# Performance work log

Hardware: AMD Instinct MI355X
Metric: run time of the kernel (lower is better)

## Reference

```python
import jax, jax.numpy as jnp
import numpy as np

N_NODES = 50000
N_RAND_EDGES = 800000
N_GRAPHS = 64
IN_DIM, HID, HEADS = 1024, 64, 4
NEG_SLOPE = 0.2  # PyG GATConv default


def setup_inputs() -> dict:
    key = jax.random.key(0)
    ks = jax.random.split(key, 16)
    x = jax.random.normal(ks[0], (N_NODES, IN_DIM), dtype=jnp.float32)
    src = jax.random.randint(ks[1], (N_RAND_EDGES,), 0, N_NODES, dtype=jnp.int32)
    dst = jax.random.randint(ks[2], (N_RAND_EDGES,), 0, N_NODES, dtype=jnp.int32)
    loop = jnp.arange(N_NODES, dtype=jnp.int32)
    # PyG GATConv adds self-loops by default; bake them into edge_index.
    edge_index = jnp.stack([jnp.concatenate([src, loop]), jnp.concatenate([dst, loop])])
    batch = jnp.sort(jax.random.randint(ks[3], (N_NODES,), 0, N_GRAPHS, dtype=jnp.int32))
    s = 0.05
    W1 = jax.random.normal(ks[4], (IN_DIM, HEADS * HID), dtype=jnp.float32) * s
    att_src1 = jax.random.normal(ks[5], (HEADS, HID), dtype=jnp.float32) * s
    att_dst1 = jax.random.normal(ks[6], (HEADS, HID), dtype=jnp.float32) * s
    b1 = jnp.zeros((HEADS * HID,), dtype=jnp.float32)
    W2 = jax.random.normal(ks[7], (HEADS * HID, HID), dtype=jnp.float32) * s
    att_src2 = jax.random.normal(ks[8], (1, HID), dtype=jnp.float32) * s
    att_dst2 = jax.random.normal(ks[9], (1, HID), dtype=jnp.float32) * s
    b2 = jnp.zeros((HID,), dtype=jnp.float32)
    fc_w = jax.random.normal(ks[10], (HID, 2), dtype=jnp.float32) * s
    fc_b = jnp.zeros((2,), dtype=jnp.float32)
    return {"x": x, "edge_index": edge_index, "batch": batch,
            "W1": W1, "att_src1": att_src1, "att_dst1": att_dst1, "b1": b1,
            "W2": W2, "att_src2": att_src2, "att_dst2": att_dst2, "b2": b2,
            "fc_w": fc_w, "fc_b": fc_b}


def gat_conv(x, src, dst, W, a_src, a_dst, b):
    """PyG GATConv (eval mode, concat=True). x:[N,Fin] -> [N, H*C]."""
    N = x.shape[0]
    H, C = a_src.shape
    h = (x @ W).reshape(N, H, C)                      # [N,H,C]
    al_s = jnp.einsum('nhc,hc->nh', h, a_src)         # [N,H]
    al_d = jnp.einsum('nhc,hc->nh', h, a_dst)
    e = jax.nn.leaky_relu(al_s[src] + al_d[dst], NEG_SLOPE)   # [E,H]
    # segment-softmax over edges grouped by destination node
    m = jax.ops.segment_max(e, dst, num_segments=N)           # [N,H]
    w = jnp.exp(e - m[dst])
    denom = jax.ops.segment_sum(w, dst, num_segments=N)
    alpha = w / denom[dst]                                    # [E,H]
    msg = h[src] * alpha[:, :, None]                          # [E,H,C]
    out = jax.ops.segment_sum(msg, dst, num_segments=N)       # [N,H,C]
    return out.reshape(N, H * C) + b


def reference(x, edge_index, batch, W1, att_src1, att_dst1, b1,
              W2, att_src2, att_dst2, b2, fc_w, fc_b):
    src, dst = edge_index[0], edge_index[1]
    # dropout is identity in eval mode
    h = jax.nn.elu(gat_conv(x, src, dst, W1, att_src1, att_dst1, b1))
    h = jax.nn.elu(gat_conv(h, src, dst, W2, att_src2, att_dst2, b2))
    # global mean pool over graphs
    sums = jax.ops.segment_sum(h, batch, num_segments=N_GRAPHS)          # [G,HID]
    cnt = jax.ops.segment_sum(jnp.ones((h.shape[0],), h.dtype), batch,
                              num_segments=N_GRAPHS)
    pooled = sums / jnp.maximum(cnt, 1.0)[:, None]
    return pooled @ fc_w + fc_b                                          # [G,2]
```

## Files before the change

### kernel.cpp

```cpp
#include <hip/hip_runtime.h>
#include <hip/hip_bf16.h>

#define NNODES   50000
#define NGRAPHS  64
#define INDIM    1024
#define HIDC     64
#define HEADS1   4
#define F1       (HEADS1*HIDC)
#define NEG_SLOPE 0.2f

#define WS_COUNTS   0
#define WS_ZEROLEN  50000
#define WS_INDPTR   54208
#define WS_CURSOR   104256
#define WS_CSRSRC   154304
#define WS_CSRDST   1004304
#define WS_BSUM     1854304
#define WS_ALS1     1854368
#define WS_ALD1     2054368
#define WS_ALS2     2254368
#define WS_ALD2     2304368
#define WS_BP       2354368
#define WS_BP2      2485440
#define WS_H1B      2493632
#define WS_X2B      8893632
#define WS_H2B      15293632
#define WS_HFIN     16893632

typedef __attribute__((ext_vector_type(8))) short bf16x8;
typedef __attribute__((ext_vector_type(4))) float f32x4;

__device__ __forceinline__ ushort f2bf(float f) {
    union { float f; uint u; } v; v.f = f;
    uint r = v.u + 0x7fff + ((v.u >> 16) & 1);
    return (ushort)(r >> 16);
}
__device__ __forceinline__ float bf2f(ushort u) {
    union { uint u; float f; } v; v.u = (uint)u << 16; return v.f;
}

__global__ void prep_kernel(const float* __restrict__ W1, const float* __restrict__ W2,
                            ushort* __restrict__ Bp1, ushort* __restrict__ Bp2,
                            int* __restrict__ counts) {
    int b = blockIdx.x;
    int tid = threadIdx.x;
    if (b < 1024) {
        int o = b * 256 + tid;
        int j = o & 7;
        int lane = (o >> 3) & 63;
        int kchunk = (o >> 9) & 31;
        int ntile = o >> 14;
        int k = kchunk * 32 + (lane >> 4) * 8 + j;
        int n = ntile * 16 + (lane & 15);
        Bp1[o] = f2bf(W1[k * 256 + n]);
    } else if (b < 1088) {
        int o = (b - 1024) * 256 + tid;
        int j = o & 7;
        int lane = (o >> 3) & 63;
        int kchunk = (o >> 9) & 7;
        int ntile = o >> 12;
        int k = kchunk * 32 + (lane >> 4) * 8 + j;
        int n = ntile * 16 + (lane & 15);
        Bp2[o] = f2bf(W2[k * 64 + n]);
    } else {
        int i = (b - 1088) * 256 + tid;
        if (i < NNODES) counts[i] = 0;
    }
}

__global__ void hist_kernel(const int* __restrict__ dst, int* __restrict__ counts, int E) {
    int i = blockIdx.x * blockDim.x + threadIdx.x;
    if (i < E) atomicAdd(&counts[dst[i]], 1);
}

__global__ __launch_bounds__(1024) void scan1_kernel(const int* __restrict__ counts,
                                                     int* __restrict__ indptr,
                                                     int* __restrict__ bsum, int N) {
    __shared__ int sm[1024];
    int b = blockIdx.x;
    int i = b * 1024 + (int)threadIdx.x;
    int v = (i < N) ? counts[i] : 0;
    sm[threadIdx.x] = v;
    __syncthreads();
    for (int off = 1; off < 1024; off <<= 1) {
        int t = (threadIdx.x >= (unsigned)off) ? sm[threadIdx.x - off] : 0;
        __syncthreads();
        sm[threadIdx.x] += t;
        __syncthreads();
    }
    if (i < N) indptr[i + 1] = sm[threadIdx.x];
    if (threadIdx.x == 1023) bsum[b] = sm[1023];
}

__global__ void scan2_kernel(int* __restrict__ bsum, int nb) {
    int lane = threadIdx.x;
    int v = (lane < nb) ? bsum[lane] : 0;
    int orig = v;
    #pragma unroll
    for (int off = 1; off < 64; off <<= 1) {
        int t = __shfl_up(v, off, 64);
        if (lane >= off) v += t;
    }
    if (lane < nb) bsum[lane] = v - orig;
}

__global__ __launch_bounds__(1024) void scan3_kernel(const int* __restrict__ counts,
                                                     int* __restrict__ indptr,
                                                     int* __restrict__ cursor,
                                                     const int* __restrict__ bsum, int N) {
    int i = blockIdx.x * 1024 + (int)threadIdx.x;
    if (i == 0) indptr[0] = 0;
    if (i < N) {
        int incl = indptr[i + 1] + bsum[blockIdx.x];
        indptr[i + 1] = incl;
        cursor[i] = incl - counts[i];
    }
}

__global__ void fill_kernel(const int* __restrict__ src, const int* __restrict__ dst,
                            int* __restrict__ cursor, int* __restrict__ csr_src, int E) {
    int i = blockIdx.x * blockDim.x + threadIdx.x;
    if (i < E) {
        int d = dst[i];
        int pos = atomicAdd(&cursor[d], 1);
        csr_src[pos] = src[i];
    }
}

__global__ __launch_bounds__(256) void gemm1_mfma(const float* __restrict__ A,
                                                  const ushort* __restrict__ Bp,
                                                  ushort* __restrict__ C,
                                                  const float* __restrict__ asrc,
                                                  const float* __restrict__ adst,
                                                  float* __restrict__ als,
                                                  float* __restrict__ ald,
                                                  int M) {
    __shared__ __align__(16) ushort Atile[2][64 * 32];
    const int K = 1024, N = 256;
    int tid = threadIdx.x;
    int lane = tid & 63;
    int w = tid >> 6;
    int wm = w >> 1, wn = w & 1;
    int m0 = blockIdx.x * 64;

    const float* srow[2];
    int soff[2];
    #pragma unroll
    for (int l = 0; l < 2; ++l) {
        int slot = l * 256 + tid;
        int m = slot >> 3, hc = slot & 7;
        int c = hc >> 1;
        int row = m0 + m; if (row >= M) row = M - 1;
        srow[l] = A + (size_t)row * K + hc * 4;
        soff[l] = (m * 4 + (c ^ ((m >> 1) & 3))) * 8 + (hc & 1) * 4;
    }
    int afrag_off[2];
    #pragma unroll
    for (int mt = 0; mt < 2; ++mt) {
        int r = wm * 32 + mt * 16 + (lane & 15);
        int cq = lane >> 4;
        afrag_off[mt] = (r * 4 + (cq ^ ((r >> 1) & 3))) * 8;
    }
    const ushort* bbase[8];
    #pragma unroll
    for (int nt = 0; nt < 8; ++nt) {
        int ntile = wn * 8 + nt;
        bbase[nt] = Bp + ((size_t)(ntile * 32) * 64 + lane) * 8;
    }

    f32x4 acc[2][8] = {};
    float4 v[2];
    #pragma unroll
    for (int l = 0; l < 2; ++l) v[l] = *(const float4*)(srow[l]);

    for (int kc = 0; kc < 32; ++kc) {
        ushort* At = Atile[kc & 1];
        #pragma unroll
        for (int l = 0; l < 2; ++l) {
            ushort4 b;
            b.x = f2bf(v[l].x); b.y = f2bf(v[l].y);
            b.z = f2bf(v[l].z); b.w = f2bf(v[l].w);
            *(ushort4*)&At[soff[l]] = b;
        }
        __syncthreads();
        if (kc < 31) {
            #pragma unroll
            for (int l = 0; l < 2; ++l)
                v[l] = *(const float4*)(srow[l] + (kc + 1) * 32);
        }
        bf16x8 afr[2];
        #pragma unroll
        for (int mt = 0; mt < 2; ++mt)
            afr[mt] = *(const bf16x8*)&At[afrag_off[mt]];
        #pragma unroll
        for (int nt = 0; nt < 8; ++nt) {
            bf16x8 bfr = *(const bf16x8*)(bbase[nt] + (size_t)kc * 64 * 8);
            #pragma unroll
            for (int mt = 0; mt < 2; ++mt)
                acc[mt][nt] = __builtin_amdgcn_mfma_f32_16x16x32_bf16(afr[mt], bfr, acc[mt][nt], 0, 0, 0);
        }
    }

    float a_s[8], a_d[8];
    #pragma unroll
    for (int nt = 0; nt < 8; ++nt) {
        int col = wn * 128 + nt * 16 + (lane & 15);
        a_s[nt] = asrc[col];
        a_d[nt] = adst[col];
    }
    #pragma unroll
    for (int mt = 0; mt < 2; ++mt) {
        #pragma unroll
        for (int nt = 0; nt < 8; ++nt) {
            int col = wn * 128 + nt * 16 + (lane & 15);
            #pragma unroll
            for (int r = 0; r < 4; ++r) {
                int row = m0 + wm * 32 + mt * 16 + (lane >> 4) * 4 + r;
                if (row < M) C[(size_t)row * N + col] = f2bf(acc[mt][nt][r]);
            }
        }
        #pragma unroll
        for (int hg = 0; hg < 2; ++hg) {
            int head = wn * 2 + hg;
            #pragma unroll
            for (int r = 0; r < 4; ++r) {
                int row = m0 + wm * 32 + mt * 16 + (lane >> 4) * 4 + r;
                float s = 0.f, d = 0.f;
                #pragma unroll
                for (int q = 0; q < 4; ++q) {
                    float c = acc[mt][4 * hg + q][r];
                    s = fmaf(c, a_s[4 * hg + q], s);
                    d = fmaf(c, a_d[4 * hg + q], d);
                }
                #pragma unroll
                for (int off = 1; off < 16; off <<= 1) {
                    s += __shfl_xor(s, off, 64);
                    d += __shfl_xor(d, off, 64);
                }
                if ((lane & 15) == 0 && row < M) {
                    als[row * 4 + head] = s;
                    ald[row * 4 + head] = d;
                }
            }
        }
    }
}

__global__ __launch_bounds__(256) void gemm2_mfma(const ushort* __restrict__ Ab,
                                                  const ushort* __restrict__ Bp,
                                                  ushort* __restrict__ C,
                                                  const float* __restrict__ asrc,
                                                  const float* __restrict__ adst,
                                                  float* __restrict__ als,
                                                  float* __restrict__ ald,
                                                  int M) {
    int tid = threadIdx.x;
    int lane = tid & 63;
    int w = tid >> 6;
    int m0 = blockIdx.x * 64 + w * 16;

    f32x4 acc[4] = {};
    #pragma unroll 2
    for (int kc = 0; kc < 8; ++kc) {
        int r = m0 + (lane & 15);
        if (r >= M) r = M - 1;
        bf16x8 afr = *(const bf16x8*)&Ab[(size_t)r * 256 + kc * 32 + (lane >> 4) * 8];
        #pragma unroll
        for (int nt = 0; nt < 4; ++nt) {
            bf16x8 bfr = *(const bf16x8*)&Bp[((nt * 8 + kc) * 64 + lane) * 8];
            acc[nt] = __builtin_amdgcn_mfma_f32_16x16x32_bf16(afr, bfr, acc[nt], 0, 0, 0);
        }
    }
    float a_s[4], a_d[4];
    #pragma unroll
    for (int nt = 0; nt < 4; ++nt) {
        a_s[nt] = asrc[nt * 16 + (lane & 15)];
        a_d[nt] = adst[nt * 16 + (lane & 15)];
    }
    #pragma unroll
    for (int nt = 0; nt < 4; ++nt) {
        int col = nt * 16 + (lane & 15);
        #pragma unroll
        for (int r = 0; r < 4; ++r) {
            int row = m0 + (lane >> 4) * 4 + r;
            if (row < M) C[(size_t)row * 64 + col] = f2bf(acc[nt][r]);
        }
    }
    #pragma unroll
    for (int r = 0; r < 4; ++r) {
        int row = m0 + (lane >> 4) * 4 + r;
        float s = 0.f, d = 0.f;
        #pragma unroll
        for (int nt = 0; nt < 4; ++nt) {
            float c = acc[nt][r];
            s = fmaf(c, a_s[nt], s);
            d = fmaf(c, a_d[nt], d);
        }
        #pragma unroll
        for (int off = 1; off < 16; off <<= 1) {
            s += __shfl_xor(s, off, 64);
            d += __shfl_xor(d, off, 64);
        }
        if ((lane & 15) == 0 && row < M) {
            als[row] = s;
            ald[row] = d;
        }
    }
}

__device__ __forceinline__ float wave_reduce_sum(float v) {
    #pragma unroll
    for (int off = 32; off > 0; off >>= 1) v += __shfl_xor(v, off, 64);
    return v;
}

__device__ __forceinline__ float edge_w(float e) {
    e = (e > 0.f) ? e : NEG_SLOPE * e;
    return __expf(e);
}

__global__ __launch_bounds__(256) void agg1_kernel(const ushort* __restrict__ h,
                                                   const float* __restrict__ als,
                                                   const float* __restrict__ ald,
                                                   const int* __restrict__ indptr,
                                                   const int* __restrict__ csr_src,
                                                   const float* __restrict__ bias,
                                                   ushort* __restrict__ out, int N) {
    __shared__ int   s_s[4][64];
    __shared__ float s_w[4][64][4];
    int wv   = threadIdx.x >> 6;
    int lane = threadIdx.x & 63;
    int n = blockIdx.x * 4 + wv;
    if (n >= N) return;
    int hd = lane >> 4;
    int beg = indptr[n], end = indptr[n + 1];
    float4 aldv = *(const float4*)&ald[n * 4];

    float4 acc = make_float4(0.f, 0.f, 0.f, 0.f);
    float den = 0.f;

    for (int base = beg; base < end; base += 64) {
        int cnt = end - base; if (cnt > 64) cnt = 64;
        if (lane < cnt) {
            int s = csr_src[base + lane];
            s_s[wv][lane] = s;
            float4 av = *(const float4*)&als[s * 4];
            s_w[wv][lane][0] = edge_w(av.x + aldv.x);
            s_w[wv][lane][1] = edge_w(av.y + aldv.y);
            s_w[wv][lane][2] = edge_w(av.z + aldv.z);
            s_w[wv][lane][3] = edge_w(av.w + aldv.w);
        }
        #pragma unroll 4
        for (int e = 0; e < cnt; ++e) {
            int s = s_s[wv][e];
            float wt = s_w[wv][e][hd];
            ushort4 a = *(const ushort4*)&h[(size_t)s * 256 + lane * 4];
            acc.x = fmaf(wt, bf2f(a.x), acc.x);
            acc.y = fmaf(wt, bf2f(a.y), acc.y);
            acc.z = fmaf(wt, bf2f(a.z), acc.z);
            acc.w = fmaf(wt, bf2f(a.w), acc.w);
            den += wt;
        }
    }

    float inv = 1.0f / den;
    float4 bv = *(const float4*)&bias[lane * 4];
    float o0 = acc.x * inv + bv.x, o1 = acc.y * inv + bv.y;
    float o2 = acc.z * inv + bv.z, o3 = acc.w * inv + bv.w;
    o0 = (o0 > 0.f) ? o0 : (__expf(o0) - 1.0f);
    o1 = (o1 > 0.f) ? o1 : (__expf(o1) - 1.0f);
    o2 = (o2 > 0.f) ? o2 : (__expf(o2) - 1.0f);
    o3 = (o3 > 0.f) ? o3 : (__expf(o3) - 1.0f);
    ushort4 ob; ob.x = f2bf(o0); ob.y = f2bf(o1); ob.z = f2bf(o2); ob.w = f2bf(o3);
    *(ushort4*)&out[(size_t)n * 256 + lane * 4] = ob;
}

__global__ __launch_bounds__(256) void agg2_kernel(const ushort* __restrict__ h,
                                                   const float* __restrict__ als,
                                                   const float* __restrict__ ald,
                                                   const int* __restrict__ indptr,
                                                   const int* __restrict__ csr_src,
                                                   const float* __restrict__ bias,
                                                   float* __restrict__ out, int N) {
    __shared__ int   s_s[8][32];
    __shared__ float s_w[8][32];
    int tid = threadIdx.x;
    int sl  = tid >> 5;
    int l32 = tid & 31;
    int n = blockIdx.x * 8 + sl;
    if (n >= N) return;
    int beg = indptr[n], end = indptr[n + 1];
    float ald_n = ald[n];

    float2 acc = make_float2(0.f, 0.f);
    float den = 0.f;

    for (int base = beg; base < end; base += 32) {
        int cnt = end - base; if (cnt > 32) cnt = 32;
        if (l32 < cnt) {
            int s = csr_src[base + l32];
            s_s[sl][l32] = s;
            s_w[sl][l32] = edge_w(als[s] + ald_n);
        }
        #pragma unroll 4
        for (int e = 0; e < cnt; ++e) {
            int s = s_s[sl][e];
            float wt = s_w[sl][e];
            ushort2 hv = *(const ushort2*)&h[(size_t)s * 64 + l32 * 2];
            acc.x = fmaf(wt, bf2f(hv.x), acc.x);
            acc.y = fmaf(wt, bf2f(hv.y), acc.y);
            den += wt;
        }
    }

    float inv = 1.0f / den;
    float o0 = acc.x * inv + bias[l32 * 2];
    float o1 = acc.y * inv + bias[l32 * 2 + 1];
    o0 = (o0 > 0.f) ? o0 : (__expf(o0) - 1.0f);
    o1 = (o1 > 0.f) ? o1 : (__expf(o1) - 1.0f);
    *(float2*)&out[(size_t)n * 64 + l32 * 2] = make_float2(o0, o1);
}

__global__ __launch_bounds__(256) void pool_fc_kernel(const float* __restrict__ hfin,
                                                      const int* __restrict__ batch,
                                                      const float* __restrict__ fc_w,
                                                      const float* __restrict__ fc_b,
                                                      float* __restrict__ out, int N) {
    __shared__ float lacc[4][64];
    int g = blockIdx.x;
    int beg, end;
    {
        int lo = 0, hi = N;
        while (lo < hi) { int mid = (lo + hi) >> 1; if (batch[mid] < g) lo = mid + 1; else hi = mid; }
        beg = lo;
        lo = beg; hi = N;
        while (lo < hi) { int mid = (lo + hi) >> 1; if (batch[mid] < g + 1) lo = mid + 1; else hi = mid; }
        end = lo;
    }
    int lane = threadIdx.x & 63;
    int wv = threadIdx.x >> 6;
    float acc = 0.f;
    for (int n = beg + wv; n < end; n += 4)
        acc += hfin[(size_t)n * 64 + lane];
    lacc[wv][lane] = acc;
    __syncthreads();
    if (wv == 0) {
        float s = lacc[0][lane] + lacc[1][lane] + lacc[2][lane] + lacc[3][lane];
        float cnt = fmaxf((float)(end - beg), 1.0f);
        float pooled = s / cnt;
        float p0 = wave_reduce_sum(pooled * fc_w[lane * 2 + 0]);
        float p1 = wave_reduce_sum(pooled * fc_w[lane * 2 + 1]);
        if (lane == 0) {
            out[g * 2 + 0] = p0 + fc_b[0];
            out[g * 2 + 1] = p1 + fc_b[1];
        }
    }
}

extern "C" void kernel_launch(void* const* d_in, const int* in_sizes, int n_in,
                              void* d_out, int out_size, void* d_ws, size_t ws_size,
                              hipStream_t stream) {
    const float* x      = (const float*)d_in[0];
    const int*   ei     = (const int*)d_in[1];
    const int*   batch  = (const int*)d_in[2];
    const float* W1     = (const float*)d_in[3];
    const float* asrc1  = (const float*)d_in[4];
    const float* adst1  = (const float*)d_in[5];
    const float* b1     = (const float*)d_in[6];
    const float* W2     = (const float*)d_in[7];
    const float* asrc2  = (const float*)d_in[8];
    const float* adst2  = (const float*)d_in[9];
    const float* b2     = (const float*)d_in[10];
    const float* fc_w   = (const float*)d_in[11];
    const float* fc_b   = (const float*)d_in[12];
    float* out          = (float*)d_out;

    const int N = in_sizes[2];
    const int E = in_sizes[1] / 2;
    const int* src = ei;
    const int* dst = ei + E;

    float* ws = (float*)d_ws;
    int*    counts  = (int*)(ws + WS_COUNTS);
    int*    indptr  = (int*)(ws + WS_INDPTR);
    int*    cursor  = (int*)(ws + WS_CURSOR);
    int*    csr_src = (int*)(ws + WS_CSRSRC);
    int*    bsum    = (int*)(ws + WS_BSUM);
    float*  al_s1   = ws + WS_ALS1;
    float*  al_d1   = ws + WS_ALD1;
    float*  al_s2   = ws + WS_ALS2;
    float*  al_d2   = ws + WS_ALD2;
    ushort* bp      = (ushort*)(ws + WS_BP);
    ushort* bp2     = (ushort*)(ws + WS_BP2);
    ushort* h1b     = (ushort*)(ws + WS_H1B);
    ushort* x2b     = (ushort*)(ws + WS_X2B);
    ushort* h2b     = (ushort*)(ws + WS_H2B);
    float*  hfin    = ws + WS_HFIN;

    const int nb = (N + 1023) / 1024;

    prep_kernel<<<1284, 256, 0, stream>>>(W1, W2, bp, bp2, counts);
    hist_kernel<<<(E + 255) / 256, 256, 0, stream>>>(dst, counts, E);
    scan1_kernel<<<nb, 1024, 0, stream>>>(counts, indptr, bsum, N);
    scan2_kernel<<<1, 64, 0, stream>>>(bsum, nb);
    scan3_kernel<<<nb, 1024, 0, stream>>>(counts, indptr, cursor, bsum, N);
    fill_kernel<<<(E + 255) / 256, 256, 0, stream>>>(src, dst, cursor, csr_src, E);
    gemm1_mfma<<<(N + 63) / 64, 256, 0, stream>>>(
        x, bp, h1b, asrc1, adst1, al_s1, al_d1, N);
    agg1_kernel<<<(N + 3) / 4, 256, 0, stream>>>(h1b, al_s1, al_d1, indptr, csr_src, b1, x2b, N);
    gemm2_mfma<<<(N + 63) / 64, 256, 0, stream>>>(
        x2b, bp2, h2b, asrc2, adst2, al_s2, al_d2, N);
    agg2_kernel<<<(N + 7) / 8, 256, 0, stream>>>(h2b, al_s2, al_d2, indptr, csr_src, b2, hfin, N);
    pool_fc_kernel<<<NGRAPHS, 256, 0, stream>>>(hfin, batch, fc_w, fc_b, out, N);
}
```

Baseline: 602.4 us.

## Restructure gemm1 with direct global-to-LDS async loads and per-wave full-N tiles

Rewrites the first-layer GEMM so that each wave owns 32 rows and all 256 output columns, with 128 rows per block. The fp32 A tile is streamed straight into a swizzled, double-buffered per-wave LDS region using global_load_lds, with explicit vmcnt waits in place of block-wide barriers. The fp32-to-bf16 conversion moves to fragment-read time. This aims to overlap A loading with MFMA and to drop the register round-trip and __syncthreads, but it doubles the accumulator registers (launch bounds 256,2), which may limit occupancy.

```diff
diff --git a/kernel.cpp b/kernel.cpp
--- a/kernel.cpp
+++ b/kernel.cpp
@@ -29,6 +29,9 @@
 
 typedef __attribute__((ext_vector_type(8))) short bf16x8;
 typedef __attribute__((ext_vector_type(4))) float f32x4;
+
+typedef __attribute__((address_space(1))) const unsigned int cgu32;
+typedef __attribute__((address_space(3))) unsigned int su32;
 
 __device__ __forceinline__ ushort f2bf(float f) {
     union { float f; uint u; } v; v.f = f;
@@ -127,7 +130,7 @@
     }
 }
 
-__global__ __launch_bounds__(256) void gemm1_mfma(const float* __restrict__ A,
+__global__ __launch_bounds__(256, 2) void gemm1_mfma(const float* __restrict__ A,
                                                   const ushort* __restrict__ Bp,
                                                   ushort* __restrict__ C,
                                                   const float* __restrict__ asrc,
@@ -135,96 +138,106 @@
                                                   float* __restrict__ als,
                                                   float* __restrict__ ald,
                                                   int M) {
-    __shared__ __align__(16) ushort Atile[2][64 * 32];
+    __shared__ __align__(16) float As[4][2][1024];
     const int K = 1024, N = 256;
     int tid = threadIdx.x;
     int lane = tid & 63;
     int w = tid >> 6;
-    int wm = w >> 1, wn = w & 1;
-    int m0 = blockIdx.x * 64;
-
-    const float* srow[2];
-    int soff[2];
-    #pragma unroll
-    for (int l = 0; l < 2; ++l) {
-        int slot = l * 256 + tid;
-        int m = slot >> 3, hc = slot & 7;
-        int c = hc >> 1;
-        int row = m0 + m; if (row >= M) row = M - 1;
-        srow[l] = A + (size_t)row * K + hc * 4;
-        soff[l] = (m * 4 + (c ^ ((m >> 1) & 3))) * 8 + (hc & 1) * 4;
-    }
-    int afrag_off[2];
+    int m0 = blockIdx.x * 128 + w * 32;
+
+    const float* gsrc[4];
+    #pragma unroll
+    for (int j = 0; j < 4; ++j) {
+        int prow = j * 8 + (lane >> 3);
+        int grow = m0 + prow; if (grow >= M) grow = M - 1;
+        int kswz = ((lane & 7) ^ (lane >> 3)) << 2;
+        gsrc[j] = A + (size_t)grow * K + kswz;
+    }
+    char* sbase = (char*)&As[w][0][0];
+
+    int aoff[2][2];
     #pragma unroll
     for (int mt = 0; mt < 2; ++mt) {
-        int r = wm * 32 + mt * 16 + (lane & 15);
-        int cq = lane >> 4;
-        afrag_off[mt] = (r * 4 + (cq ^ ((r >> 1) & 3))) * 8;
-    }
-    const ushort* bbase[8];
-    #pragma unroll
-    for (int nt = 0; nt < 8; ++nt) {
-        int ntile = wn * 8 + nt;
-        bbase[nt] = Bp + ((size_t)(ntile * 32) * 64 + lane) * 8;
-    }
-
-    f32x4 acc[2][8] = {};
-    float4 v[2];
-    #pragma unroll
-    for (int l = 0; l < 2; ++l) v[l] = *(const float4*)(srow[l]);
-
-    for (int kc = 0; kc < 32; ++kc) {
-        ushort* At = Atile[kc & 1];
-        #pragma unroll
-        for (int l = 0; l < 2; ++l) {
-            ushort4 b;
-            b.x = f2bf(v[l].x); b.y = f2bf(v[l].y);
-            b.z = f2bf(v[l].z); b.w = f2bf(v[l].w);
-            *(ushort4*)&At[soff[l]] = b;
-        }
-        __syncthreads();
-        if (kc < 31) {
-            #pragma unroll
-            for (int l = 0; l < 2; ++l)
-                v[l] = *(const float4*)(srow[l] + (kc + 1) * 32);
-        }
-        bf16x8 afr[2];
-        #pragma unroll
-        for (int mt = 0; mt < 2; ++mt)
-            afr[mt] = *(const bf16x8*)&At[afrag_off[mt]];
-        #pragma unroll
-        for (int nt = 0; nt < 8; ++nt) {
-            bf16x8 bfr = *(const bf16x8*)(bbase[nt] + (size_t)kc * 64 * 8);
-            #pragma unroll
-            for (int mt = 0; mt < 2; ++mt)
-                acc[mt][nt] = __builtin_amdgcn_mfma_f32_16x16x32_bf16(afr[mt], bfr, acc[mt][nt], 0, 0, 0);
-        }
-    }
-
-    float a_s[8], a_d[8];
-    #pragma unroll
-    for (int nt = 0; nt < 8; ++nt) {
-        int col = wn * 128 + nt * 16 + (lane & 15);
+        int lr = mt * 16 + (lane & 15);
+        int kq = lane >> 4;
+        #pragma unroll
+        for (int h = 0; h < 2; ++h)
+            aoff[mt][h] = lr * 128 + ((kq * 32 + h * 16) ^ ((lr & 7) << 4));
+    }
+
+    f32x4 acc[2][16] = {};
+
+    #pragma unroll
+    for (int j = 0; j < 4; ++j)
+        __builtin_amdgcn_global_load_lds((cgu32*)(gsrc[j]),
+                                         (su32*)(sbase + j * 1024 + lane * 16), 16, 0, 0);
+
+    #define G1_BLOADS(kc_)                                                          \
+        bf16x8 bfr[16];                                                             \
+        _Pragma("unroll")                                                           \
+        for (int nt = 0; nt < 16; ++nt)                                             \
+            bfr[nt] = *(const bf16x8*)&Bp[((size_t)(nt * 32 + (kc_)) * 64 + lane) * 8];
+    #define G1_FRAGS_MFMA(kc_)                                                      \
+        const char* sb = sbase + ((kc_) & 1) * 4096;                                \
+        bf16x8 afr[2];                                                              \
+        _Pragma("unroll")                                                           \
+        for (int mt = 0; mt < 2; ++mt) {                                            \
+            float4 fa = *(const float4*)(sb + aoff[mt][0]);                         \
+            float4 fb = *(const float4*)(sb + aoff[mt][1]);                         \
+            bf16x8 t;                                                               \
+            t[0] = (short)f2bf(fa.x); t[1] = (short)f2bf(fa.y);                     \
+            t[2] = (short)f2bf(fa.z); t[3] = (short)f2bf(fa.w);                     \
+            t[4] = (short)f2bf(fb.x); t[5] = (short)f2bf(fb.y);                     \
+            t[6] = (short)f2bf(fb.z); t[7] = (short)f2bf(fb.w);                     \
+            afr[mt] = t;                                                            \
+        }                                                                           \
+        _Pragma("unroll")                                                           \
+        for (int nt = 0; nt < 16; ++nt) {                                           \
+            acc[0][nt] = __builtin_amdgcn_mfma_f32_16x16x32_bf16(afr[0], bfr[nt], acc[0][nt], 0, 0, 0); \
+            acc[1][nt] = __builtin_amdgcn_mfma_f32_16x16x32_bf16(afr[1], bfr[nt], acc[1][nt], 0, 0, 0); \
+        }
+
+    for (int kc = 0; kc < 31; ++kc) {
+        G1_BLOADS(kc);
+        char* sn = sbase + ((kc + 1) & 1) * 4096;
+        #pragma unroll
+        for (int j = 0; j < 4; ++j)
+            __builtin_amdgcn_global_load_lds((cgu32*)(gsrc[j] + (kc + 1) * 32),
+                                             (su32*)(sn + j * 1024 + lane * 16), 16, 0, 0);
+        asm volatile("s_waitcnt vmcnt(4)" ::: "memory");
+        G1_FRAGS_MFMA(kc);
+    }
+    {
+        G1_BLOADS(31);
+        asm volatile("s_waitcnt vmcnt(0)" ::: "memory");
+        G1_FRAGS_MFMA(31);
+    }
+    #undef G1_BLOADS
+    #undef G1_FRAGS_MFMA
+
+    float a_s[16], a_d[16];
+    #pragma unroll
+    for (int nt = 0; nt < 16; ++nt) {
+        int col = nt * 16 + (lane & 15);
         a_s[nt] = asrc[col];
         a_d[nt] = adst[col];
     }
     #pragma unroll
     for (int mt = 0; mt < 2; ++mt) {
         #pragma unroll
-        for (int nt = 0; nt < 8; ++nt) {
-            int col = wn * 128 + nt * 16 + (lane & 15);
+        for (int nt = 0; nt < 16; ++nt) {
+            int col = nt * 16 + (lane & 15);
             #pragma unroll
             for (int r = 0; r < 4; ++r) {
-                int row = m0 + wm * 32 + mt * 16 + (lane >> 4) * 4 + r;
+                int row = m0 + mt * 16 + (lane >> 4) * 4 + r;
                 if (row < M) C[(size_t)row * N + col] = f2bf(acc[mt][nt][r]);
             }
         }
         #pragma unroll
-        for (int hg = 0; hg < 2; ++hg) {
-            int head = wn * 2 + hg;
+        for (int hg = 0; hg < 4; ++hg) {
             #pragma unroll
             for (int r = 0; r < 4; ++r) {
-                int row = m0 + wm * 32 + mt * 16 + (lane >> 4) * 4 + r;
+                int row = m0 + mt * 16 + (lane >> 4) * 4 + r;
                 float s = 0.f, d = 0.f;
                 #pragma unroll
                 for (int q = 0; q < 4; ++q) {
@@ -238,8 +251,8 @@
                     d += __shfl_xor(d, off, 64);
                 }
                 if ((lane & 15) == 0 && row < M) {
-                    als[row * 4 + head] = s;
-                    ald[row * 4 + head] = d;
+                    als[row * 4 + hg] = s;
+                    ald[row * 4 + hg] = d;
                 }
             }
         }
@@ -505,7 +518,7 @@
     scan2_kernel<<<1, 64, 0, stream>>>(bsum, nb);
     scan3_kernel<<<nb, 1024, 0, stream>>>(counts, indptr, cursor, bsum, N);
     fill_kernel<<<(E + 255) / 256, 256, 0, stream>>>(src, dst, cursor, csr_src, E);
-    gemm1_mfma<<<(N + 63) / 64, 256, 0, stream>>>(
+    gemm1_mfma<<<(N + 127) / 128, 256, 0, stream>>>(
         x, bp, h1b, asrc1, adst1, al_s1, al_d1, N);
     agg1_kernel<<<(N + 3) / 4, 256, 0, stream>>>(h1b, al_s1, al_d1, indptr, csr_src, b1, x2b, N);
     gemm2_mfma<<<(N + 63) / 64, 256, 0, stream>>>(
```

Result: no change. 602.0 us (-0.1%).

## Stage GEMM1 A and B tiles into LDS via async global_load_lds

Applied to the files above, without the earlier changes.

Rewrites the first-layer GEMM main loop so both the fp32 A tile and the pre-packed bf16 B tile are copied into double-buffered shared memory with direct global-to-LDS loads, overlapping the next chunk's fetch with the current chunk's MFMAs. The fp32-to-bf16 conversion moves to after the LDS read and uses packed convert instructions. An XOR swizzle on A is meant to avoid bank conflicts, and launch bounds request 3 blocks per CU. The cost is larger LDS use per block (fp32 A plus B buffers), which may limit occupancy, and the barrier placement relies on the async loads having completed.

```diff
diff --git a/kernel.cpp b/kernel.cpp
--- a/kernel.cpp
+++ b/kernel.cpp
@@ -30,6 +30,9 @@
 typedef __attribute__((ext_vector_type(8))) short bf16x8;
 typedef __attribute__((ext_vector_type(4))) float f32x4;
 
+typedef __attribute__((address_space(1))) const unsigned int cgu32;
+typedef __attribute__((address_space(3))) unsigned int su32;
+
 __device__ __forceinline__ ushort f2bf(float f) {
     union { float f; uint u; } v; v.f = f;
     uint r = v.u + 0x7fff + ((v.u >> 16) & 1);
@@ -37,6 +40,11 @@
 }
 __device__ __forceinline__ float bf2f(ushort u) {
     union { uint u; float f; } v; v.u = (uint)u << 16; return v.f;
+}
+__device__ __forceinline__ uint cvtpk(float lo, float hi) {
+    uint r;
+    asm("v_cvt_pk_bf16_f32 %0, %1, %2" : "=v"(r) : "v"(lo), "v"(hi));
+    return r;
 }
 
 __global__ void prep_kernel(const float* __restrict__ W1, const float* __restrict__ W2,
@@ -127,7 +135,7 @@
     }
 }
 
-__global__ __launch_bounds__(256) void gemm1_mfma(const float* __restrict__ A,
+__global__ __launch_bounds__(256, 3) void gemm1_mfma(const float* __restrict__ A,
                                                   const ushort* __restrict__ Bp,
                                                   ushort* __restrict__ C,
                                                   const float* __restrict__ asrc,
@@ -135,7 +143,8 @@
                                                   float* __restrict__ als,
                                                   float* __restrict__ ald,
                                                   int M) {
-    __shared__ __align__(16) ushort Atile[2][64 * 32];
+    __shared__ __align__(16) float  As[2][2048];
+    __shared__ __align__(16) ushort Bs[2][8192];
     const int K = 1024, N = 256;
     int tid = threadIdx.x;
     int lane = tid & 63;
@@ -143,63 +152,82 @@
     int wm = w >> 1, wn = w & 1;
     int m0 = blockIdx.x * 64;
 
-    const float* srow[2];
-    int soff[2];
-    #pragma unroll
-    for (int l = 0; l < 2; ++l) {
-        int slot = l * 256 + tid;
-        int m = slot >> 3, hc = slot & 7;
-        int c = hc >> 1;
-        int row = m0 + m; if (row >= M) row = M - 1;
-        srow[l] = A + (size_t)row * K + hc * 4;
-        soff[l] = (m * 4 + (c ^ ((m >> 1) & 3))) * 8 + (hc & 1) * 4;
-    }
-    int afrag_off[2];
+    const float* gsrcA[2];
+    #pragma unroll
+    for (int j = 0; j < 2; ++j) {
+        int gidx = j * 256 + tid;
+        int r = gidx >> 3, c = gidx & 7;
+        int grow = m0 + r; if (grow >= M) grow = M - 1;
+        gsrcA[j] = A + (size_t)grow * K + ((c ^ (r & 7)) << 2);
+    }
+    const ushort* gsrcB[4];
+    #pragma unroll
+    for (int j = 0; j < 4; ++j) {
+        int nt = j * 4 + w;
+        gsrcB[j] = Bp + (size_t)nt * 16384 + lane * 8;
+    }
+
+    int aoffA[2][2];
     #pragma unroll
     for (int mt = 0; mt < 2; ++mt) {
-        int r = wm * 32 + mt * 16 + (lane & 15);
-        int cq = lane >> 4;
-        afrag_off[mt] = (r * 4 + (cq ^ ((r >> 1) & 3))) * 8;
-    }
-    const ushort* bbase[8];
-    #pragma unroll
-    for (int nt = 0; nt < 8; ++nt) {
-        int ntile = wn * 8 + nt;
-        bbase[nt] = Bp + ((size_t)(ntile * 32) * 64 + lane) * 8;
-    }
+        int row = wm * 32 + mt * 16 + (lane & 15);
+        int kq = lane >> 4;
+        aoffA[mt][0] = row * 128 + (((kq * 2)     ^ (row & 7)) << 4);
+        aoffA[mt][1] = row * 128 + (((kq * 2 + 1) ^ (row & 7)) << 4);
+    }
+    int boff[8];
+    #pragma unroll
+    for (int nt = 0; nt < 8; ++nt)
+        boff[nt] = (wn * 8 + nt) * 1024 + lane * 16;
 
     f32x4 acc[2][8] = {};
-    float4 v[2];
-    #pragma unroll
-    for (int l = 0; l < 2; ++l) v[l] = *(const float4*)(srow[l]);
-
-    for (int kc = 0; kc < 32; ++kc) {
-        ushort* At = Atile[kc & 1];
-        #pragma unroll
-        for (int l = 0; l < 2; ++l) {
-            ushort4 b;
-            b.x = f2bf(v[l].x); b.y = f2bf(v[l].y);
-            b.z = f2bf(v[l].z); b.w = f2bf(v[l].w);
-            *(ushort4*)&At[soff[l]] = b;
-        }
+
+    auto STAGE = [&](int buf, int kc) {
+        char* da = (char*)As[buf];
+        char* db = (char*)Bs[buf];
+        #pragma unroll
+        for (int j = 0; j < 2; ++j)
+            __builtin_amdgcn_global_load_lds((cgu32*)(gsrcA[j] + kc * 32),
+                                             (su32*)(da + j * 4096 + tid * 16), 16, 0, 0);
+        #pragma unroll
+        for (int j = 0; j < 4; ++j)
+            __builtin_amdgcn_global_load_lds((cgu32*)(gsrcB[j] + kc * 512),
+                                             (su32*)(db + j * 4096 + tid * 16), 16, 0, 0);
+    };
+    auto COMPUTE = [&](int buf) {
+        const char* sa = (const char*)As[buf];
+        const char* sb = (const char*)Bs[buf];
+        bf16x8 afr[2];
+        #pragma unroll
+        for (int mt = 0; mt < 2; ++mt) {
+            float4 fa = *(const float4*)(sa + aoffA[mt][0]);
+            float4 fb = *(const float4*)(sa + aoffA[mt][1]);
+            union { uint u[4]; bf16x8 v; } p;
+            p.u[0] = cvtpk(fa.x, fa.y);
+            p.u[1] = cvtpk(fa.z, fa.w);
+            p.u[2] = cvtpk(fb.x, fb.y);
+            p.u[3] = cvtpk(fb.z, fb.w);
+            afr[mt] = p.v;
+        }
+        bf16x8 bfr[8];
+        #pragma unroll
+        for (int nt = 0; nt < 8; ++nt)
+            bfr[nt] = *(const bf16x8*)(sb + boff[nt]);
+        #pragma unroll
+        for (int nt = 0; nt < 8; ++nt) {
+            acc[0][nt] = __builtin_amdgcn_mfma_f32_16x16x32_bf16(afr[0], bfr[nt], acc[0][nt], 0, 0, 0);
+            acc[1][nt] = __builtin_amdgcn_mfma_f32_16x16x32_bf16(afr[1], bfr[nt], acc[1][nt], 0, 0, 0);
+        }
+    };
+
+    STAGE(0, 0);
+    __syncthreads();
+    for (int kc = 0; kc < 31; ++kc) {
+        STAGE((kc + 1) & 1, kc + 1);
+        COMPUTE(kc & 1);
         __syncthreads();
-        if (kc < 31) {
-            #pragma unroll
-            for (int l = 0; l < 2; ++l)
-                v[l] = *(const float4*)(srow[l] + (kc + 1) * 32);
-        }
-        bf16x8 afr[2];
-        #pragma unroll
-        for (int mt = 0; mt < 2; ++mt)
-            afr[mt] = *(const bf16x8*)&At[afrag_off[mt]];
-        #pragma unroll
-        for (int nt = 0; nt < 8; ++nt) {
-            bf16x8 bfr = *(const bf16x8*)(bbase[nt] + (size_t)kc * 64 * 8);
-            #pragma unroll
-            for (int mt = 0; mt < 2; ++mt)
-                acc[mt][nt] = __builtin_amdgcn_mfma_f32_16x16x32_bf16(afr[mt], bfr, acc[mt][nt], 0, 0, 0);
-        }
-    }
+    }
+    COMPUTE(1);
 
     float a_s[8], a_d[8];
     #pragma unroll
```

Result: no change. 613.7 us (+1.9%).

## Restructure gemm1 A staging into 128-wide K slabs with deeper prefetch

Applied to the files above, without the earlier changes.

gemm1 now stages 128-wide K slabs of A into double-buffered LDS, using an XOR swizzle and packed bf16 conversion via v_cvt_pk_bf16_f32. Global loads are prefetched two groups ahead, and synchronisation uses raw s_barrier only once per 4 k-steps. This is meant to cut barrier count and conversion instructions and to hide more global latency. It costs more registers (16 float4 prefetch buffers) with launch_bounds set to 2 blocks per SM, and 32KB of LDS. The aggregation kernels also raise their edge-loop unroll from 4 to 8.

```diff
diff --git a/kernel.cpp b/kernel.cpp
--- a/kernel.cpp
+++ b/kernel.cpp
@@ -38,6 +38,12 @@
 __device__ __forceinline__ float bf2f(ushort u) {
     union { uint u; float f; } v; v.u = (uint)u << 16; return v.f;
 }
+__device__ __forceinline__ uint cvtpk(float lo, float hi) {
+    uint r;
+    asm("v_cvt_pk_bf16_f32 %0, %1, %2" : "=v"(r) : "v"(lo), "v"(hi));
+    return r;
+}
+#define RAW_BARRIER() asm volatile("s_waitcnt lgkmcnt(0)\n\ts_barrier" ::: "memory")
 
 __global__ void prep_kernel(const float* __restrict__ W1, const float* __restrict__ W2,
                             ushort* __restrict__ Bp1, ushort* __restrict__ Bp2,
@@ -127,7 +133,7 @@
     }
 }
 
-__global__ __launch_bounds__(256) void gemm1_mfma(const float* __restrict__ A,
+__global__ __launch_bounds__(256, 2) void gemm1_mfma(const float* __restrict__ A,
                                                   const ushort* __restrict__ Bp,
                                                   ushort* __restrict__ C,
                                                   const float* __restrict__ asrc,
@@ -135,7 +141,7 @@
                                                   float* __restrict__ als,
                                                   float* __restrict__ ald,
                                                   int M) {
-    __shared__ __align__(16) ushort Atile[2][64 * 32];
+    __shared__ __align__(16) ushort Asl[2][64 * 128];
     const int K = 1024, N = 256;
     int tid = threadIdx.x;
     int lane = tid & 63;
@@ -143,63 +149,88 @@
     int wm = w >> 1, wn = w & 1;
     int m0 = blockIdx.x * 64;
 
-    const float* srow[2];
-    int soff[2];
-    #pragma unroll
-    for (int l = 0; l < 2; ++l) {
-        int slot = l * 256 + tid;
-        int m = slot >> 3, hc = slot & 7;
-        int c = hc >> 1;
-        int row = m0 + m; if (row >= M) row = M - 1;
-        srow[l] = A + (size_t)row * K + hc * 4;
-        soff[l] = (m * 4 + (c ^ ((m >> 1) & 3))) * 8 + (hc & 1) * 4;
-    }
-    int afrag_off[2];
+    int rloc = tid >> 2, q = tid & 3;
+    int grow = m0 + rloc; if (grow >= M) grow = M - 1;
+    const float* gA = A + (size_t)grow * K + q * 32;
+
+    char* abase = (char*)&Asl[0][0];
+    int woff[4];
+    #pragma unroll
+    for (int j = 0; j < 4; ++j)
+        woff[j] = rloc * 256 + (((q * 4 + j) ^ (rloc & 15)) << 4);
+
+    int aoff[2][4];
     #pragma unroll
     for (int mt = 0; mt < 2; ++mt) {
         int r = wm * 32 + mt * 16 + (lane & 15);
-        int cq = lane >> 4;
-        afrag_off[mt] = (r * 4 + (cq ^ ((r >> 1) & 3))) * 8;
+        int kq = lane >> 4;
+        #pragma unroll
+        for (int s = 0; s < 4; ++s)
+            aoff[mt][s] = r * 256 + (((s * 4 + kq) ^ (r & 15)) << 4);
     }
     const ushort* bbase[8];
     #pragma unroll
-    for (int nt = 0; nt < 8; ++nt) {
-        int ntile = wn * 8 + nt;
-        bbase[nt] = Bp + ((size_t)(ntile * 32) * 64 + lane) * 8;
-    }
+    for (int nt = 0; nt < 8; ++nt)
+        bbase[nt] = Bp + ((size_t)((wn * 8 + nt) * 32) * 64 + lane) * 8;
 
     f32x4 acc[2][8] = {};
-    float4 v[2];
-    #pragma unroll
-    for (int l = 0; l < 2; ++l) v[l] = *(const float4*)(srow[l]);
-
-    for (int kc = 0; kc < 32; ++kc) {
-        ushort* At = Atile[kc & 1];
-        #pragma unroll
-        for (int l = 0; l < 2; ++l) {
-            ushort4 b;
-            b.x = f2bf(v[l].x); b.y = f2bf(v[l].y);
-            b.z = f2bf(v[l].z); b.w = f2bf(v[l].w);
-            *(ushort4*)&At[soff[l]] = b;
-        }
-        __syncthreads();
-        if (kc < 31) {
-            #pragma unroll
-            for (int l = 0; l < 2; ++l)
-                v[l] = *(const float4*)(srow[l] + (kc + 1) * 32);
-        }
-        bf16x8 afr[2];
-        #pragma unroll
-        for (int mt = 0; mt < 2; ++mt)
-            afr[mt] = *(const bf16x8*)&At[afrag_off[mt]];
-        #pragma unroll
-        for (int nt = 0; nt < 8; ++nt) {
-            bf16x8 bfr = *(const bf16x8*)(bbase[nt] + (size_t)kc * 64 * 8);
-            #pragma unroll
-            for (int mt = 0; mt < 2; ++mt)
-                acc[mt][nt] = __builtin_amdgcn_mfma_f32_16x16x32_bf16(afr[mt], bfr, acc[mt][nt], 0, 0, 0);
-        }
-    }
+    float4 vA[8], vB[8];
+
+    #define G1_LOAD(V, G)                                                     \
+        _Pragma("unroll")                                                     \
+        for (int j = 0; j < 8; ++j)                                           \
+            V[j] = *(const float4*)(gA + (G) * 128 + j * 4);
+    #define G1_WRITE(V, PAR)                                                  \
+        {                                                                     \
+            char* dw = abase + (PAR) * 16384;                                 \
+            _Pragma("unroll")                                                 \
+            for (int j = 0; j < 4; ++j) {                                     \
+                uint4 t;                                                      \
+                t.x = cvtpk(V[2*j].x,   V[2*j].y);                            \
+                t.y = cvtpk(V[2*j].z,   V[2*j].w);                            \
+                t.z = cvtpk(V[2*j+1].x, V[2*j+1].y);                          \
+                t.w = cvtpk(V[2*j+1].z, V[2*j+1].w);                          \
+                *(uint4*)(dw + woff[j]) = t;                                  \
+            }                                                                 \
+        }
+    #define G1_GROUP(G, VWR, VLD)                                             \
+        {                                                                     \
+            const char* sb = abase + ((G) & 1) * 16384;                       \
+            _Pragma("unroll")                                                 \
+            for (int s = 0; s < 4; ++s) {                                     \
+                int kc = (G) * 4 + s;                                         \
+                bf16x8 bfr[8];                                                \
+                _Pragma("unroll")                                             \
+                for (int nt = 0; nt < 8; ++nt)                                \
+                    bfr[nt] = *(const bf16x8*)(bbase[nt] + (size_t)kc * 512); \
+                bf16x8 afr[2];                                                \
+                _Pragma("unroll")                                             \
+                for (int mt = 0; mt < 2; ++mt)                                \
+                    afr[mt] = *(const bf16x8*)(sb + aoff[mt][s]);             \
+                _Pragma("unroll")                                             \
+                for (int nt = 0; nt < 8; ++nt) {                              \
+                    acc[0][nt] = __builtin_amdgcn_mfma_f32_16x16x32_bf16(afr[0], bfr[nt], acc[0][nt], 0, 0, 0); \
+                    acc[1][nt] = __builtin_amdgcn_mfma_f32_16x16x32_bf16(afr[1], bfr[nt], acc[1][nt], 0, 0, 0); \
+                }                                                             \
+            }                                                                 \
+            RAW_BARRIER();                    \
+            if ((G) < 7) G1_WRITE(VWR, ((G) + 1) & 1);                        \
+            if ((G) < 6) G1_LOAD(VLD, (G) + 2);                               \
+            if ((G) < 7) RAW_BARRIER();           \
+        }
+
+    G1_LOAD(vA, 0);
+    G1_WRITE(vA, 0);
+    G1_LOAD(vB, 1);
+    RAW_BARRIER();
+    #pragma unroll
+    for (int g = 0; g < 8; g += 2) {
+        G1_GROUP(g,     vB, vA);
+        G1_GROUP(g + 1, vA, vB);
+    }
+    #undef G1_LOAD
+    #undef G1_WRITE
+    #undef G1_GROUP
 
     float a_s[8], a_d[8];
     #pragma unroll
@@ -227,10 +258,10 @@
                 int row = m0 + wm * 32 + mt * 16 + (lane >> 4) * 4 + r;
                 float s = 0.f, d = 0.f;
                 #pragma unroll
-                for (int q = 0; q < 4; ++q) {
-                    float c = acc[mt][4 * hg + q][r];
-                    s = fmaf(c, a_s[4 * hg + q], s);
-                    d = fmaf(c, a_d[4 * hg + q], d);
+                for (int qq = 0; qq < 4; ++qq) {
+                    float c = acc[mt][4 * hg + qq][r];
+                    s = fmaf(c, a_s[4 * hg + qq], s);
+                    d = fmaf(c, a_d[4 * hg + qq], d);
                 }
                 #pragma unroll
                 for (int off = 1; off < 16; off <<= 1) {
@@ -350,7 +381,7 @@
             s_w[wv][lane][2] = edge_w(av.z + aldv.z);
             s_w[wv][lane][3] = edge_w(av.w + aldv.w);
         }
-        #pragma unroll 4
+        #pragma unroll 8
         for (int e = 0; e < cnt; ++e) {
             int s = s_s[wv][e];
             float wt = s_w[wv][e][hd];
@@ -402,7 +433,7 @@
             s_s[sl][l32] = s;
             s_w[sl][l32] = edge_w(als[s] + ald_n);
         }
-        #pragma unroll 4
+        #pragma unroll 8
         for (int e = 0; e < cnt; ++e) {
             int s = s_s[sl][e];
             float wt = s_w[sl][e];
```

After: 658.7 us. 9.4% more time.
